# Performance work log

Measured on AMD Instinct MI355X. Metric: run time of the kernel, lower is better.

The kernel has to match this reference:

```python
import jax, jax.numpy as jnp
import numpy as np

N, E, IN, OUT, R, B = 20000, 640000, 256, 800, 8, 8


def setup_inputs() -> dict:
    key = jax.random.key(0)
    k0, k1, k2, k3, k4, k5 = jax.random.split(key, 6)
    x = jax.random.normal(k0, (N, IN), dtype=jnp.float32)
    edge_index = jax.random.randint(k1, (2, E), 0, N, dtype=jnp.int32)
    edge_type = jax.random.randint(k2, (E,), 0, R, dtype=jnp.int32)
    # basis-decomposed relation weights: W_r = sum_b att[r,b] * bases[b]
    bases = jax.random.normal(k3, (B, IN, OUT), dtype=jnp.float32) * 0.05
    att = jax.random.normal(k4, (R, B), dtype=jnp.float32) * 0.3
    root = jax.random.normal(k5, (IN, OUT), dtype=jnp.float32) * 0.05
    bias = jnp.zeros((OUT,), dtype=jnp.float32)
    return {"x": x, "edge_index": edge_index, "edge_type": edge_type,
            "bases": bases, "att": att, "root": root, "bias": bias}


def reference(x, edge_index, edge_type, bases, att, root, bias):
    # RGCNConv (basis decomposition, scatter-add aggregation):
    #   out[v] = sum_{(u->v, r) in edges} x[u] @ W_r  +  x[v] @ root  +  bias
    # Efficient form: first segment-sum x[src] per (dst, relation), then one
    # dense contraction with the R relation weights (math-identical for add-aggr).
    n, in_dim = x.shape
    r, b = att.shape
    W = jnp.einsum('rb,bio->rio', att, bases)          # [R, IN, OUT]
    src, dst = edge_index[0], edge_index[1]
    seg = dst.astype(jnp.int32) * r + edge_type.astype(jnp.int32)
    # per-(node, relation) sums of source features: [N*R, IN] -> [N, R, IN]
    s = jax.ops.segment_sum(x[src], seg, num_segments=n * r).reshape(n, r, in_dim)
    out = jnp.einsum('nri,rio->no', s, W) + x @ root + bias
    return out
```

## Files before the change

kernel.cpp:

```cpp
#include <hip/hip_runtime.h>


#define N_NODES 20000
#define N_EDGES 640000
#define IN_DIM  256
#define OUT_DIM 800
#define NREL    8
#define NSEG    160000
#define KS      2048
#define KTOT    2304
#define NPAD    1024
#define NB      625

#define BM 256
#define BN 160
#define BK 64
#define NKT (KTOT / BK)
#define MT  79
#define NT  5
#define NWG (MT * NT)
#define ABYTES 32768
#define LBUF 53248

#define XCAST_B (N_NODES * 64 / 256)
#define WCAT_B  ((KTOT / 8) * 4)
#define INIT_NWG (NB + XCAST_B + WCAT_B)

typedef float f32x4_t __attribute__((ext_vector_type(4)));
typedef short short8_t __attribute__((ext_vector_type(8)));

__device__ __forceinline__ unsigned short f2bf(float f) {
  unsigned u = __float_as_uint(f);
  u += 0x7fffu + ((u >> 16) & 1u);
  return (unsigned short)(u >> 16);
}

__device__ __forceinline__ float bflo(unsigned w) { return __uint_as_float(w << 16); }
__device__ __forceinline__ float bfhi(unsigned w) { return __uint_as_float(w & 0xffff0000u); }

__device__ __forceinline__ void gload16(const void* g, void* l) {
  __builtin_amdgcn_global_load_lds(
      (const __attribute__((address_space(1))) void*)g,
      (__attribute__((address_space(3))) void*)l, 16, 0, 0);
}

__global__ void init_kernel(const float* __restrict__ x,
                            const float* __restrict__ bases,
                            const float* __restrict__ att,
                            const float* __restrict__ root,
                            int* __restrict__ cnt,
                            unsigned short* __restrict__ abf,
                            unsigned short* __restrict__ wcatT,
                            int* __restrict__ gtotal) {
  const int b = blockIdx.x;
  const int t = threadIdx.x;
  if (b < NB) {
    cnt[b * 256 + t] = 0;
    if (b == 0 && t == 0) *gtotal = 0;
  } else if (b < NB + XCAST_B) {
    const int id = (b - NB) * 256 + t;
    const int row = id >> 6, lane = id & 63;
    const float4 v = ((const float4*)x)[(size_t)row * 64 + lane];
    union { unsigned short u[4]; uint2 q; } pk;
    pk.u[0] = f2bf(v.x); pk.u[1] = f2bf(v.y);
    pk.u[2] = f2bf(v.z); pk.u[3] = f2bf(v.w);
    *(uint2*)(abf + (size_t)row * KTOT + KS + lane * 4) = pk.q;
  } else {
    const int rem = b - NB - XCAST_B;
    const int kc = rem >> 2, ng = rem & 3;
    const int k0 = kc * 8;
    const int n  = ng * 256 + t;
    if (n >= OUT_DIM) return;
    union { unsigned short u[8]; uint4 q; } pk;
    if (k0 < KS) {
      const int r = k0 >> 8, i0 = k0 & 255;
      float av[8];
      #pragma unroll
      for (int bb = 0; bb < 8; ++bb) av[bb] = att[r * 8 + bb];
      #pragma unroll
      for (int j = 0; j < 8; ++j) {
        float v = 0.f;
        #pragma unroll
        for (int bb = 0; bb < 8; ++bb)
          v += av[bb] * bases[((size_t)bb * IN_DIM + i0 + j) * OUT_DIM + n];
        pk.u[j] = f2bf(v);
      }
    } else {
      #pragma unroll
      for (int j = 0; j < 8; ++j)
        pk.u[j] = f2bf(root[(size_t)(k0 - KS + j) * OUT_DIM + n]);
    }
    *(uint4*)(wcatT + (size_t)n * KTOT + k0) = pk.q;
  }
}


__global__ void hist_kernel(const int* __restrict__ ei, const int* __restrict__ et,
                            int* __restrict__ cnt) {
  const int e0 = (blockIdx.x * 256 + threadIdx.x) * 4;
  const int4 d = *(const int4*)(ei + N_EDGES + e0);
  const int4 r = *(const int4*)(et + e0);
  atomicAdd(&cnt[d.x * NREL + r.x], 1);
  atomicAdd(&cnt[d.y * NREL + r.y], 1);
  atomicAdd(&cnt[d.z * NREL + r.z], 1);
  atomicAdd(&cnt[d.w * NREL + r.w], 1);
}

__global__ void alloc_kernel(const int* __restrict__ cnt, int* __restrict__ off,
                             int* __restrict__ cur, int* __restrict__ gtotal) {
  __shared__ int sm[256];
  __shared__ int sbase;
  const int t = threadIdx.x;
  const int g = blockIdx.x * 256 + t;
  const int v = cnt[g];
  sm[t] = v;
  __syncthreads();
  for (int s = 1; s < 256; s <<= 1) {
    const int a = (t >= s) ? sm[t - s] : 0;
    __syncthreads();
    sm[t] += a;
    __syncthreads();
  }
  if (t == 255) sbase = atomicAdd(gtotal, sm[255]);
  __syncthreads();
  const int ex = sm[t] - v + sbase;
  off[g] = ex;
  cur[g] = ex;
}

__global__ void reorder_kernel(const int* __restrict__ ei, const int* __restrict__ et,
                               int* __restrict__ cur, int* __restrict__ sorted_src) {
  const int e0 = (blockIdx.x * 256 + threadIdx.x) * 4;
  const int4 s = *(const int4*)(ei + e0);
  const int4 d = *(const int4*)(ei + N_EDGES + e0);
  const int4 r = *(const int4*)(et + e0);
  sorted_src[atomicAdd(&cur[d.x * NREL + r.x], 1)] = s.x;
  sorted_src[atomicAdd(&cur[d.y * NREL + r.y], 1)] = s.y;
  sorted_src[atomicAdd(&cur[d.z * NREL + r.z], 1)] = s.z;
  sorted_src[atomicAdd(&cur[d.w * NREL + r.w], 1)] = s.w;
}

__global__ void aggregate_kernel(const int* __restrict__ cnt, const int* __restrict__ off,
                                 const int* __restrict__ sorted_src,
                                 unsigned short* __restrict__ abf) {
  const int seg = __builtin_amdgcn_readfirstlane(blockIdx.x * 4 + (threadIdx.x >> 6));
  const int l = threadIdx.x & 63;
  const int half = l >> 5;
  const int sl = l & 31;
  const int ne = cnt[seg];
  const int o  = off[seg];
  float a0 = 0.f, a1 = 0.f, a2 = 0.f, a3 = 0.f;
  float a4 = 0.f, a5 = 0.f, a6 = 0.f, a7 = 0.f;
  int j = 0;
  for (; j + 2 <= ne; j += 2) {
    const int s = sorted_src[o + j + half];
    const uint4 u = *(const uint4*)(abf + (size_t)s * KTOT + KS + sl * 8);
    a0 += bflo(u.x); a1 += bfhi(u.x); a2 += bflo(u.y); a3 += bfhi(u.y);
    a4 += bflo(u.z); a5 += bfhi(u.z); a6 += bflo(u.w); a7 += bfhi(u.w);
  }
  if (j < ne && half == 0) {
    const int s = sorted_src[o + j];
    const uint4 u = *(const uint4*)(abf + (size_t)s * KTOT + KS + sl * 8);
    a0 += bflo(u.x); a1 += bfhi(u.x); a2 += bflo(u.y); a3 += bfhi(u.y);
    a4 += bflo(u.z); a5 += bfhi(u.z); a6 += bflo(u.w); a7 += bfhi(u.w);
  }
  a0 += __shfl_xor(a0, 32); a1 += __shfl_xor(a1, 32);
  a2 += __shfl_xor(a2, 32); a3 += __shfl_xor(a3, 32);
  a4 += __shfl_xor(a4, 32); a5 += __shfl_xor(a5, 32);
  a6 += __shfl_xor(a6, 32); a7 += __shfl_xor(a7, 32);
  if (half == 0) {
    const int node = seg >> 3, r = seg & 7;
    union { unsigned short u[8]; uint4 q; } pk;
    pk.u[0] = f2bf(a0); pk.u[1] = f2bf(a1); pk.u[2] = f2bf(a2); pk.u[3] = f2bf(a3);
    pk.u[4] = f2bf(a4); pk.u[5] = f2bf(a5); pk.u[6] = f2bf(a6); pk.u[7] = f2bf(a7);
    *(uint4*)(abf + (size_t)node * KTOT + r * IN_DIM + sl * 8) = pk.q;
  }
}

__global__ __launch_bounds__(512) void gemm_kernel(
    const unsigned short* __restrict__ abf,
    const unsigned short* __restrict__ wcatT,
    const float* __restrict__ bias, float* __restrict__ out) {
  __shared__ __align__(16) char lds[3 * LBUF];

  const int lin = blockIdx.x;
  const int q8 = NWG >> 3, r8 = NWG & 7;
  const int xcd = lin & 7, idx = lin >> 3;
  const int wg = (xcd < r8 ? xcd * (q8 + 1) : r8 * (q8 + 1) + (xcd - r8) * q8) + idx;
  const int row0 = (wg / NT) * BM;
  const int col0 = (wg % NT) * BN;

  const int tid = threadIdx.x;
  const int w = tid >> 6, l = tid & 63;
  const int wm = w >> 1, wn = w & 1;
  const int la = l & 15, lg = l >> 4;
  const int l3 = l >> 3;
  const int sch = (l & 7) ^ l3;

  const unsigned short* gA[4];
  #pragma unroll
  for (int i = 0; i < 4; ++i) {
    int ga = row0 + i * 64 + w * 8 + l3;
    ga = (ga < N_NODES) ? ga : (N_NODES - 1);
    gA[i] = abf + (size_t)ga * KTOT + sch * 8;
  }
  const int b2row = (w < 4) ? (128 + w * 8 + l3) : ((w - 4) * 8 + l3);
  const unsigned short* gB0 = wcatT + (size_t)(col0 + w * 8 + l3) * KTOT + sch * 8;
  const unsigned short* gB1 = wcatT + (size_t)(col0 + 64 + w * 8 + l3) * KTOT + sch * 8;
  const unsigned short* gB2 = wcatT + (size_t)(col0 + b2row) * KTOT + sch * 8;
  const int dB2 = (w < 4) ? (ABYTES + 16384 + w * 1024) : (ABYTES + (w - 4) * 1024);

  f32x4_t acc[4][5];
  #pragma unroll
  for (int i = 0; i < 4; ++i)
    #pragma unroll
    for (int j = 0; j < 5; ++j)
      acc[i][j] = (f32x4_t)(0.0f);

  auto stage_all = [&](int buf, int kt) {
    char* base = lds + buf * LBUF;
    const int ko = kt * BK;
    gload16(gA[0] + ko, base + w * 1024);
    gload16(gA[1] + ko, base + 8192 + w * 1024);
    gload16(gA[2] + ko, base + 16384 + w * 1024);
    gload16(gA[3] + ko, base + 24576 + w * 1024);
    gload16(gB0 + ko, base + ABYTES + w * 1024);
    gload16(gB1 + ko, base + ABYTES + 8192 + w * 1024);
    gload16(gB2 + ko, base + dB2);
  };

  stage_all(0, 0);
  stage_all(1, 1);

  for (int kt = 0; kt < NKT; ++kt) {
    const int cbuf = kt % 3;
    const int pbuf = (kt + 2) % 3;
    const bool pf = (kt + 2) < NKT;
    const int pko = (kt + 2) * BK;
    const char* Ab = lds + cbuf * LBUF;
    const char* Bb = Ab + ABYTES;
    char* pbase = lds + pbuf * LBUF;

    if (kt + 1 < NKT) { asm volatile("s_waitcnt vmcnt(7)" ::: "memory"); }
    else              { asm volatile("s_waitcnt vmcnt(0)" ::: "memory"); }
    __builtin_amdgcn_sched_barrier(0);
    __builtin_amdgcn_s_barrier();

    short8_t af0, af1, bfv[5];

    {
      const int r0 = wm * 64 + la, r1 = wm * 64 + 16 + la;
      af0 = *(const short8_t*)(Ab + r0 * 128 + ((lg << 4) ^ ((r0 & 7) << 4)));
      af1 = *(const short8_t*)(Ab + r1 * 128 + ((lg << 4) ^ ((r1 & 7) << 4)));
      #pragma unroll
      for (int nf = 0; nf < 5; ++nf) {
        const int rr = wn * 80 + nf * 16 + la;
        bfv[nf] = *(const short8_t*)(Bb + rr * 128 + ((lg << 4) ^ ((rr & 7) << 4)));
      }
      if (pf) { gload16(gA[0] + pko, pbase + w * 1024);
                gload16(gA[1] + pko, pbase + 8192 + w * 1024); }
      __builtin_amdgcn_s_barrier();
      asm volatile("s_waitcnt lgkmcnt(0)" ::: "memory");
      __builtin_amdgcn_sched_barrier(0);
      __builtin_amdgcn_s_setprio(1);
      #pragma unroll
      for (int nf = 0; nf < 5; ++nf)
        acc[0][nf] = __builtin_amdgcn_mfma_f32_16x16x32_bf16(af0, bfv[nf], acc[0][nf], 0, 0, 0);
      #pragma unroll
      for (int nf = 0; nf < 5; ++nf)
        acc[1][nf] = __builtin_amdgcn_mfma_f32_16x16x32_bf16(af1, bfv[nf], acc[1][nf], 0, 0, 0);
      __builtin_amdgcn_s_setprio(0);
      __builtin_amdgcn_s_barrier();
    }
    {
      const int r0 = wm * 64 + 32 + la, r1 = wm * 64 + 48 + la;
      af0 = *(const short8_t*)(Ab + r0 * 128 + ((lg << 4) ^ ((r0 & 7) << 4)));
      af1 = *(const short8_t*)(Ab + r1 * 128 + ((lg << 4) ^ ((r1 & 7) << 4)));
      if (pf) { gload16(gA[2] + pko, pbase + 16384 + w * 1024);
                gload16(gA[3] + pko, pbase + 24576 + w * 1024); }
      __builtin_amdgcn_s_barrier();
      asm volatile("s_waitcnt lgkmcnt(0)" ::: "memory");
      __builtin_amdgcn_sched_barrier(0);
      __builtin_amdgcn_s_setprio(1);
      #pragma unroll
      for (int nf = 0; nf < 5; ++nf)
        acc[2][nf] = __builtin_amdgcn_mfma_f32_16x16x32_bf16(af0, bfv[nf], acc[2][nf], 0, 0, 0);
      #pragma unroll
      for (int nf = 0; nf < 5; ++nf)
        acc[3][nf] = __builtin_amdgcn_mfma_f32_16x16x32_bf16(af1, bfv[nf], acc[3][nf], 0, 0, 0);
      __builtin_amdgcn_s_setprio(0);
      __builtin_amdgcn_s_barrier();
    }
    {
      const int r0 = wm * 64 + la, r1 = wm * 64 + 16 + la;
      af0 = *(const short8_t*)(Ab + r0 * 128 + (((4 + lg) << 4) ^ ((r0 & 7) << 4)));
      af1 = *(const short8_t*)(Ab + r1 * 128 + (((4 + lg) << 4) ^ ((r1 & 7) << 4)));
      #pragma unroll
      for (int nf = 0; nf < 5; ++nf) {
        const int rr = wn * 80 + nf * 16 + la;
        bfv[nf] = *(const short8_t*)(Bb + rr * 128 + (((4 + lg) << 4) ^ ((rr & 7) << 4)));
      }
      if (pf) { gload16(gB0 + pko, pbase + ABYTES + w * 1024);
                gload16(gB1 + pko, pbase + ABYTES + 8192 + w * 1024); }
      __builtin_amdgcn_s_barrier();
      asm volatile("s_waitcnt lgkmcnt(0)" ::: "memory");
      __builtin_amdgcn_sched_barrier(0);
      __builtin_amdgcn_s_setprio(1);
      #pragma unroll
      for (int nf = 0; nf < 5; ++nf)
        acc[0][nf] = __builtin_amdgcn_mfma_f32_16x16x32_bf16(af0, bfv[nf], acc[0][nf], 0, 0, 0);
      #pragma unroll
      for (int nf = 0; nf < 5; ++nf)
        acc[1][nf] = __builtin_amdgcn_mfma_f32_16x16x32_bf16(af1, bfv[nf], acc[1][nf], 0, 0, 0);
      __builtin_amdgcn_s_setprio(0);
      __builtin_amdgcn_s_barrier();
    }
    {
      const int r0 = wm * 64 + 32 + la, r1 = wm * 64 + 48 + la;
      af0 = *(const short8_t*)(Ab + r0 * 128 + (((4 + lg) << 4) ^ ((r0 & 7) << 4)));
      af1 = *(const short8_t*)(Ab + r1 * 128 + (((4 + lg) << 4) ^ ((r1 & 7) << 4)));
      if (pf) { gload16(gB2 + pko, pbase + dB2); }
      __builtin_amdgcn_s_barrier();
      asm volatile("s_waitcnt lgkmcnt(0)" ::: "memory");
      __builtin_amdgcn_sched_barrier(0);
      __builtin_amdgcn_s_setprio(1);
      #pragma unroll
      for (int nf = 0; nf < 5; ++nf)
        acc[2][nf] = __builtin_amdgcn_mfma_f32_16x16x32_bf16(af0, bfv[nf], acc[2][nf], 0, 0, 0);
      #pragma unroll
      for (int nf = 0; nf < 5; ++nf)
        acc[3][nf] = __builtin_amdgcn_mfma_f32_16x16x32_bf16(af1, bfv[nf], acc[3][nf], 0, 0, 0);
      __builtin_amdgcn_s_setprio(0);
      __builtin_amdgcn_s_barrier();
    }
  }

  #pragma unroll
  for (int nf = 0; nf < 5; ++nf) {
    const int gcol = col0 + wn * 80 + nf * 16 + la;
    const float bv = bias[gcol];
    #pragma unroll
    for (int f = 0; f < 4; ++f) {
      const int gr0 = row0 + wm * 64 + f * 16 + lg * 4;
      #pragma unroll
      for (int j = 0; j < 4; ++j) {
        const int gr = gr0 + j;
        if (gr < N_NODES)
          out[(size_t)gr * OUT_DIM + gcol] = acc[f][nf][j] + bv;
      }
    }
  }
}

extern "C" void kernel_launch(void* const* d_in, const int* in_sizes, int n_in,
                              void* d_out, int out_size, void* d_ws, size_t ws_size,
                              hipStream_t stream) {
  const float* x     = (const float*)d_in[0];
  const int*   ei    = (const int*)d_in[1];
  const int*   et    = (const int*)d_in[2];
  const float* bases = (const float*)d_in[3];
  const float* att   = (const float*)d_in[4];
  const float* root  = (const float*)d_in[5];
  const float* bias  = (const float*)d_in[6];
  float* out = (float*)d_out;

  char* p = (char*)d_ws;
  unsigned short* abf   = (unsigned short*)p;  p += (size_t)N_NODES * KTOT * 2;
  unsigned short* wcatT = (unsigned short*)p;  p += (size_t)NPAD * KTOT * 2;
  int* cnt        = (int*)p;                   p += (size_t)NSEG * 4;
  int* off        = (int*)p;                   p += (size_t)NSEG * 4;
  int* cur        = (int*)p;                   p += (size_t)NSEG * 4;
  int* sorted_src = (int*)p;                   p += (size_t)N_EDGES * 4;
  int* gtotal     = (int*)p;                   p += 4096;

  init_kernel<<<INIT_NWG, 256, 0, stream>>>(x, bases, att, root, cnt, abf, wcatT, gtotal);
  hist_kernel<<<N_EDGES / 1024, 256, 0, stream>>>(ei, et, cnt);
  alloc_kernel<<<NB, 256, 0, stream>>>(cnt, off, cur, gtotal);
  reorder_kernel<<<N_EDGES / 1024, 256, 0, stream>>>(ei, et, cur, sorted_src);
  aggregate_kernel<<<NSEG / 4, 256, 0, stream>>>(cnt, off, sorted_src, abf);
  gemm_kernel<<<NWG, 512, 0, stream>>>(abf, wcatT, bias, out);
}
```

Before: 242.6 us.

## Gather from compact bf16 x copy and process all relations per wave

```diff
diff --git a/kernel.cpp b/kernel.cpp
--- a/kernel.cpp
+++ b/kernel.cpp
@@ -51,6 +51,7 @@
                             int* __restrict__ cnt,
                             unsigned short* __restrict__ abf,
                             unsigned short* __restrict__ wcatT,
+                            unsigned short* __restrict__ xg,
                             int* __restrict__ gtotal) {
   const int b = blockIdx.x;
   const int t = threadIdx.x;
@@ -65,6 +66,7 @@
     pk.u[0] = f2bf(v.x); pk.u[1] = f2bf(v.y);
     pk.u[2] = f2bf(v.z); pk.u[3] = f2bf(v.w);
     *(uint2*)(abf + (size_t)row * KTOT + KS + lane * 4) = pk.q;
+    *(uint2*)(xg + (size_t)row * IN_DIM + lane * 4) = pk.q;
   } else {
     const int rem = b - NB - XCAST_B;
     const int kc = rem >> 2, ng = rem & 3;
@@ -142,38 +144,53 @@
 
 __global__ void aggregate_kernel(const int* __restrict__ cnt, const int* __restrict__ off,
                                  const int* __restrict__ sorted_src,
+                                 const unsigned short* __restrict__ xg,
                                  unsigned short* __restrict__ abf) {
-  const int seg = __builtin_amdgcn_readfirstlane(blockIdx.x * 4 + (threadIdx.x >> 6));
+  const int dst = __builtin_amdgcn_readfirstlane(blockIdx.x * 4 + (threadIdx.x >> 6));
   const int l = threadIdx.x & 63;
   const int half = l >> 5;
   const int sl = l & 31;
-  const int ne = cnt[seg];
-  const int o  = off[seg];
-  float a0 = 0.f, a1 = 0.f, a2 = 0.f, a3 = 0.f;
-  float a4 = 0.f, a5 = 0.f, a6 = 0.f, a7 = 0.f;
-  int j = 0;
-  for (; j + 2 <= ne; j += 2) {
-    const int s = sorted_src[o + j + half];
-    const uint4 u = *(const uint4*)(abf + (size_t)s * KTOT + KS + sl * 8);
-    a0 += bflo(u.x); a1 += bfhi(u.x); a2 += bflo(u.y); a3 += bfhi(u.y);
-    a4 += bflo(u.z); a5 += bfhi(u.z); a6 += bflo(u.w); a7 += bfhi(u.w);
-  }
-  if (j < ne && half == 0) {
-    const int s = sorted_src[o + j];
-    const uint4 u = *(const uint4*)(abf + (size_t)s * KTOT + KS + sl * 8);
-    a0 += bflo(u.x); a1 += bfhi(u.x); a2 += bflo(u.y); a3 += bfhi(u.y);
-    a4 += bflo(u.z); a5 += bfhi(u.z); a6 += bflo(u.w); a7 += bfhi(u.w);
-  }
-  a0 += __shfl_xor(a0, 32); a1 += __shfl_xor(a1, 32);
-  a2 += __shfl_xor(a2, 32); a3 += __shfl_xor(a3, 32);
-  a4 += __shfl_xor(a4, 32); a5 += __shfl_xor(a5, 32);
-  a6 += __shfl_xor(a6, 32); a7 += __shfl_xor(a7, 32);
-  if (half == 0) {
-    const int node = seg >> 3, r = seg & 7;
-    union { unsigned short u[8]; uint4 q; } pk;
-    pk.u[0] = f2bf(a0); pk.u[1] = f2bf(a1); pk.u[2] = f2bf(a2); pk.u[3] = f2bf(a3);
-    pk.u[4] = f2bf(a4); pk.u[5] = f2bf(a5); pk.u[6] = f2bf(a6); pk.u[7] = f2bf(a7);
-    *(uint4*)(abf + (size_t)node * KTOT + r * IN_DIM + sl * 8) = pk.q;
+  unsigned short* const orow = abf + (size_t)dst * KTOT + sl * 8;
+
+  #pragma unroll 1
+  for (int r = 0; r < 8; ++r) {
+    const int ne = cnt[dst * 8 + r];
+    const int o  = off[dst * 8 + r];
+    float a0 = 0.f, a1 = 0.f, a2 = 0.f, a3 = 0.f;
+    float a4 = 0.f, a5 = 0.f, a6 = 0.f, a7 = 0.f;
+    int j = 0;
+    for (; j + 4 <= ne; j += 4) {
+      const int s0 = sorted_src[o + j + half];
+      const int s1 = sorted_src[o + j + 2 + half];
+      const uint4 u = *(const uint4*)(xg + (size_t)s0 * IN_DIM + sl * 8);
+      const uint4 v = *(const uint4*)(xg + (size_t)s1 * IN_DIM + sl * 8);
+      a0 += bflo(u.x); a1 += bfhi(u.x); a2 += bflo(u.y); a3 += bfhi(u.y);
+      a4 += bflo(u.z); a5 += bfhi(u.z); a6 += bflo(u.w); a7 += bfhi(u.w);
+      a0 += bflo(v.x); a1 += bfhi(v.x); a2 += bflo(v.y); a3 += bfhi(v.y);
+      a4 += bflo(v.z); a5 += bfhi(v.z); a6 += bflo(v.w); a7 += bfhi(v.w);
+    }
+    for (; j + 2 <= ne; j += 2) {
+      const int s = sorted_src[o + j + half];
+      const uint4 u = *(const uint4*)(xg + (size_t)s * IN_DIM + sl * 8);
+      a0 += bflo(u.x); a1 += bfhi(u.x); a2 += bflo(u.y); a3 += bfhi(u.y);
+      a4 += bflo(u.z); a5 += bfhi(u.z); a6 += bflo(u.w); a7 += bfhi(u.w);
+    }
+    if (j < ne && half == 0) {
+      const int s = sorted_src[o + j];
+      const uint4 u = *(const uint4*)(xg + (size_t)s * IN_DIM + sl * 8);
+      a0 += bflo(u.x); a1 += bfhi(u.x); a2 += bflo(u.y); a3 += bfhi(u.y);
+      a4 += bflo(u.z); a5 += bfhi(u.z); a6 += bflo(u.w); a7 += bfhi(u.w);
+    }
+    a0 += __shfl_xor(a0, 32); a1 += __shfl_xor(a1, 32);
+    a2 += __shfl_xor(a2, 32); a3 += __shfl_xor(a3, 32);
+    a4 += __shfl_xor(a4, 32); a5 += __shfl_xor(a5, 32);
+    a6 += __shfl_xor(a6, 32); a7 += __shfl_xor(a7, 32);
+    if (half == 0) {
+      union { unsigned short u[8]; uint4 q; } pk;
+      pk.u[0] = f2bf(a0); pk.u[1] = f2bf(a1); pk.u[2] = f2bf(a2); pk.u[3] = f2bf(a3);
+      pk.u[4] = f2bf(a4); pk.u[5] = f2bf(a5); pk.u[6] = f2bf(a6); pk.u[7] = f2bf(a7);
+      *(uint4*)(orow + r * IN_DIM) = pk.q;
+    }
   }
 }
 
@@ -367,16 +384,17 @@
   char* p = (char*)d_ws;
   unsigned short* abf   = (unsigned short*)p;  p += (size_t)N_NODES * KTOT * 2;
   unsigned short* wcatT = (unsigned short*)p;  p += (size_t)NPAD * KTOT * 2;
+  unsigned short* xg    = (unsigned short*)p;  p += (size_t)N_NODES * IN_DIM * 2;
   int* cnt        = (int*)p;                   p += (size_t)NSEG * 4;
   int* off        = (int*)p;                   p += (size_t)NSEG * 4;
   int* cur        = (int*)p;                   p += (size_t)NSEG * 4;
   int* sorted_src = (int*)p;                   p += (size_t)N_EDGES * 4;
   int* gtotal     = (int*)p;                   p += 4096;
 
-  init_kernel<<<INIT_NWG, 256, 0, stream>>>(x, bases, att, root, cnt, abf, wcatT, gtotal);
+  init_kernel<<<INIT_NWG, 256, 0, stream>>>(x, bases, att, root, cnt, abf, wcatT, xg, gtotal);
   hist_kernel<<<N_EDGES / 1024, 256, 0, stream>>>(ei, et, cnt);
   alloc_kernel<<<NB, 256, 0, stream>>>(cnt, off, cur, gtotal);
   reorder_kernel<<<N_EDGES / 1024, 256, 0, stream>>>(ei, et, cur, sorted_src);
-  aggregate_kernel<<<NSEG / 4, 256, 0, stream>>>(cnt, off, sorted_src, abf);
+  aggregate_kernel<<<N_NODES / 4, 256, 0, stream>>>(cnt, off, sorted_src, xg, abf);
   gemm_kernel<<<NWG, 512, 0, stream>>>(abf, wcatT, bias, out);
 }
```

New measurement: 230.8 us. -4.9%, faster.
